# Kernel optimization log

Measured on AMD Instinct MI355X. Metric: run time of the kernel, lower is better.

## Reference

```python
import jax, jax.numpy as jnp
import numpy as np

B, S, E, DQ, DV = 8, 2048, 1024, 128, 128


def setup_inputs() -> dict:
    k0 = jax.random.key(0)
    ks = jax.random.split(k0, 10)
    scale_in = 1.0 / np.sqrt(E)
    return {
        "pad_mask": jax.random.uniform(ks[0], (B, S)) < 0.1,  # True = padded key position
        "query": jax.random.normal(ks[1], (B, S, E), jnp.float32),
        "key": jax.random.normal(ks[2], (B, S, E), jnp.float32),
        "value": jax.random.normal(ks[3], (B, S, E), jnp.float32),
        "Wq": jax.random.uniform(ks[4], (E, DQ), jnp.float32, -scale_in, scale_in),
        "bq": jnp.zeros((DQ,), jnp.float32),
        "Wk": jax.random.uniform(ks[5], (E, DQ), jnp.float32, -scale_in, scale_in),
        "bk": jnp.zeros((DQ,), jnp.float32),
        "Wv": jax.random.uniform(ks[6], (E, DV), jnp.float32, -scale_in, scale_in),
        "bv": jnp.zeros((DV,), jnp.float32),
    }


def reference(pad_mask, query, key, value, Wq, bq, Wk, bk, Wv, bv):
    # Linear projections (torch Linear: x @ W^T + b; weights stored pre-transposed here)
    q = query @ Wq + bq  # [B,S,DQ]
    k = key @ Wk + bk    # [B,S,DQ]
    v = value @ Wv + bv  # [B,S,DV]

    scores = jnp.einsum("bqd,bkd->bqk", q, k)  # [B,S,S]
    # Causal mask applied BEFORE scaling (as in source); -inf/scale is still -inf
    seq = scores.shape[1]
    causal = jnp.triu(jnp.ones((seq, seq), bool), k=1)
    scores = jnp.where(causal[None], -jnp.inf, scores)
    scores = scores / jnp.asarray(q.shape[-1] ** 0.5, scores.dtype)
    # Padding mask: mask key positions with -1e9 (broadcast over query dim)
    scores = jnp.where(pad_mask[:, None, :], jnp.asarray(-1e9, scores.dtype), scores)

    attn = jax.nn.softmax(scores, axis=-1)
    return jnp.einsum("bqk,bkd->bqd", attn, v)  # [B,S,DV]
```

## Files before the change

### kernel.cpp

```cpp
#include <hip/hip_runtime.h>
#include <hip/hip_bf16.h>

#define SEQ 2048
#define EMB 1024
#define DH  128
#define QSCALE 0.08838834764831845f

typedef __attribute__((ext_vector_type(4))) float f32x4;
typedef __attribute__((ext_vector_type(8))) short bf16x8;
typedef __attribute__((ext_vector_type(4))) short bf16x4;

__device__ __forceinline__ short f2bf(float f) {
  unsigned u = __builtin_bit_cast(unsigned, f);
  u += 0x7fffu + ((u >> 16) & 1u);
  return (short)(u >> 16);
}

__device__ __forceinline__ float bf2f(short s) {
  unsigned u = ((unsigned)(unsigned short)s) << 16;
  return __builtin_bit_cast(float, u);
}

__device__ __forceinline__ f32x4 mfma16(bf16x8 a, bf16x8 b, f32x4 c) {
  return __builtin_amdgcn_mfma_f32_16x16x32_bf16(a, b, c, 0, 0, 0);
}

__device__ __forceinline__ void gl_lds16(void* lds_base, const void* gsrc) {
  __builtin_amdgcn_global_load_lds(
      (const __attribute__((address_space(1))) void*)gsrc,
      (__attribute__((address_space(3))) void*)lds_base, 16, 0, 0);
}

__global__ void prep_weights(const float* __restrict__ Wq, const float* __restrict__ Wk,
                             const float* __restrict__ Wv, short* __restrict__ wt) {
  int gid = blockIdx.x * 256 + threadIdx.x;
  int lane = gid & 63, c = lane & 15, g = (lane >> 4) & 3;
  int nb = (gid >> 6) & 7;
  int kk = (gid >> 9) & 31;
  int p = gid >> 14;
  const float* W = (p == 0) ? Wq : ((p == 1) ? Wk : Wv);
  bf16x8 v;
#pragma unroll
  for (int j = 0; j < 8; ++j)
    v[j] = f2bf(W[(kk * 32 + g * 8 + j) * DH + nb * 16 + c]);
  *(bf16x8*)(&wt[(size_t)gid * 8]) = v;
}

__global__ __launch_bounds__(256, 2) void proj_gemm(
    const float* __restrict__ Xq, const float* __restrict__ Xk, const float* __restrict__ Xv,
    const short* __restrict__ wt,
    const float* __restrict__ bq, const float* __restrict__ bk, const float* __restrict__ bv,
    short* __restrict__ qp, short* __restrict__ kp, short* __restrict__ vt) {
  __shared__ char a_lds[4][2][8192];

  const int tid = threadIdx.x;
  const int w = tid >> 6, lane = tid & 63;
  const int g = lane >> 4, c = lane & 15;
  const int bid = blockIdx.x;
  const int p = bid >> 8, mb = bid & 255;
  const int row0 = (mb << 6) + (w << 4);
  const float* X    = (p == 0) ? Xq : ((p == 1) ? Xk : Xv);
  const float* bias = (p == 0) ? bq : ((p == 1) ? bk : bv);
  const char* Xs  = (const char*)X + (size_t)row0 * 4096;
  const char* WT  = (const char*)wt + (size_t)p * 262144;

  f32x4 acc[8];
#pragma unroll
  for (int nb = 0; nb < 8; ++nb) acc[nb] = (f32x4){0.f, 0.f, 0.f, 0.f};

  bf16x8 wr[2][8];

  auto stage_A = [&](int b, int kc) {
#pragma unroll
    for (int j = 0; j < 8; ++j) {
      int r = (j << 1) + (lane >> 5);
      int off = ((lane & 31) << 4) ^ ((r & 7) << 5);
      gl_lds16(&a_lds[w][b][j * 1024],
               Xs + (size_t)r * 4096 + kc * 512 + off);
    }
  };

  auto loadW = [&](bf16x8* dst, int t) {
#pragma unroll
    for (int nb = 0; nb < 8; ++nb)
      dst[nb] = *(const bf16x8*)(WT + (size_t)t * 8192 + nb * 1024 + (lane << 4));
  };

  auto computeT = [&](const bf16x8* wf, int b, int s) {
    const char* ab = &a_lds[w][b][0];
    int ad = (c << 9) + (((s << 7) + (g << 5)) ^ ((c & 7) << 5));
    f32x4 lo = *(const f32x4*)(ab + ad);
    f32x4 hi = *(const f32x4*)(ab + ad + 16);
    bf16x8 a;
#pragma unroll
    for (int j = 0; j < 4; ++j) { a[j] = f2bf(lo[j]); a[4 + j] = f2bf(hi[j]); }
#pragma unroll
    for (int nb = 0; nb < 8; ++nb) acc[nb] = mfma16(a, wf[nb], acc[nb]);
  };

  stage_A(0, 0);
  loadW(wr[0], 0);
  __builtin_amdgcn_sched_barrier(0);

#pragma unroll
  for (int t = 0; t < 32; ++t) {
    const int s = t & 3, kc = t >> 2;
    if (s == 0 && kc < 7) stage_A((kc + 1) & 1, kc + 1);
    if (t + 1 < 32) loadW(wr[(t + 1) & 1], t + 1);
    __builtin_amdgcn_sched_barrier(0);
    if (t == 31)                       asm volatile("s_waitcnt vmcnt(0)" ::: "memory");
    else if (s == 0 && t <= 24)        asm volatile("s_waitcnt vmcnt(16)" ::: "memory");
    else                               asm volatile("s_waitcnt vmcnt(8)" ::: "memory");
    __builtin_amdgcn_sched_barrier(0);
    computeT(wr[t & 1], kc & 1, s);
    __builtin_amdgcn_sched_barrier(0);
  }

  float bvals[8];
#pragma unroll
  for (int nb = 0; nb < 8; ++nb) bvals[nb] = bias[nb * 16 + c];

  if (p < 2) {
    short* outp = (p == 0) ? qp : kp;
    float sc = (p == 0) ? QSCALE : 1.0f;
#pragma unroll
    for (int r = 0; r < 4; ++r) {
      int token = row0 + g * 4 + r;
#pragma unroll
      for (int nb = 0; nb < 8; ++nb)
        outp[token * 128 + nb * 16 + c] = f2bf((acc[nb][r] + bvals[nb]) * sc);
    }
  } else {
    int tok0 = row0 + g * 4;
    int b_ = tok0 >> 11, s_ = tok0 & 2047;
#pragma unroll
    for (int nb = 0; nb < 8; ++nb) {
      int col = nb * 16 + c;
      bf16x4 v4;
#pragma unroll
      for (int r = 0; r < 4; ++r) v4[r] = f2bf(acc[nb][r] + bvals[nb]);
      *(bf16x4*)(&vt[((size_t)(b_ * 128 + col)) * 2048 + s_]) = v4;
    }
  }
}

__global__ __launch_bounds__(256) void avgv2_kernel(
    const short* __restrict__ vt, const int* __restrict__ pad,
    const float* __restrict__ bvv, float* __restrict__ avgv) {
  int b = blockIdx.x >> 3, dg = blockIdx.x & 7;
  int t = threadIdx.x, doff = t >> 4, sl = t & 15;
  int d = dg * 16 + doff;
  const short* vrow = vt + ((size_t)(b * 128 + d)) * 2048 + sl * 128;
  const int* prow = pad + (b << 11) + sl * 128;
  float sum = 0.f;
  int cnt = 0;
  for (int i = 0; i < 16; ++i) {
    bf16x8 v8 = *(const bf16x8*)(vrow + i * 8);
#pragma unroll
    for (int j = 0; j < 8; ++j) {
      int pd = prow[i * 8 + j];
      cnt += (pd != 0);
      if (pd) sum += bf2f(v8[j]);
    }
  }
#pragma unroll
  for (int xm = 1; xm < 16; xm <<= 1) {
    sum += __shfl_xor(sum, xm, 64);
    cnt += __shfl_xor(cnt, xm, 64);
  }
  if (sl == 0) avgv[(b << 7) + d] = (cnt > 0) ? (sum / (float)cnt) : 0.f;
  (void)bvv;
}

__device__ __forceinline__ void stage_kv(short* kb, short* vb,
                                         const char* kb_base, const char* vb_base,
                                         int kt, int w, int lane) {
#pragma unroll
  for (int ch = w; ch < 16; ch += 4) {
    int phys = ch * 1024 + lane * 16;
    int lg = phys ^ (((phys >> 8) & 7) << 4);
    gl_lds16((char*)kb + ch * 1024,
             kb_base + (size_t)(kt * 64 + (lg >> 8)) * 256 + (lg & 255));
  }
#pragma unroll
  for (int ch = w; ch < 16; ch += 4) {
    int phys = ch * 1024 + lane * 16;
    int lg = phys ^ (((phys >> 7) & 7) << 4);
    gl_lds16((char*)vb + ch * 1024,
             vb_base + (size_t)(lg >> 7) * 4096 + kt * 128 + (lg & 127));
  }
}

template <bool CAUSAL>
__device__ __forceinline__ void attn_tile(
    const short* __restrict__ k_lds, const short* __restrict__ v_lds, short* __restrict__ p_w,
    const bf16x8 (&qf)[4], f32x4 (&acc_o)[8], float (&m_r)[4], float (&l_r)[4],
    const int* __restrict__ padp, int kt, int qrow_g, int g, int c) {
  f32x4 sc[4];
#pragma unroll
  for (int nb = 0; nb < 4; ++nb) sc[nb] = (f32x4){0.f, 0.f, 0.f, 0.f};
#pragma unroll
  for (int ks = 0; ks < 4; ++ks) {
    bf16x8 kf[4];
#pragma unroll
    for (int nb = 0; nb < 4; ++nb) {
      int n = (nb << 4) + c;
      int off = (n << 8) + (ks << 6) + (g << 4);
      kf[nb] = *(const bf16x8*)((const char*)k_lds + (off ^ ((n & 7) << 4)));
    }
#pragma unroll
    for (int nb = 0; nb < 4; ++nb) sc[nb] = mfma16(qf[ks], kf[nb], sc[nb]);
  }

  int padv[4];
#pragma unroll
  for (int nb = 0; nb < 4; ++nb) padv[nb] = padp[kt + (nb << 4) + c];
  float sv[4][4];
#pragma unroll
  for (int nb = 0; nb < 4; ++nb) {
    bool pd = padv[nb] != 0;
    int key = kt + (nb << 4) + c;
#pragma unroll
    for (int r = 0; r < 4; ++r) {
      float s = sc[nb][r];
      if (CAUSAL && key > qrow_g + r) s = -1e30f;
      if (pd) s = -1e30f;
      sv[nb][r] = s;
    }
  }
  float tmax[4];
#pragma unroll
  for (int r = 0; r < 4; ++r)
    tmax[r] = fmaxf(fmaxf(sv[0][r], sv[1][r]), fmaxf(sv[2][r], sv[3][r]));
#pragma unroll
  for (int xm = 1; xm < 16; xm <<= 1)
#pragma unroll
    for (int r = 0; r < 4; ++r) tmax[r] = fmaxf(tmax[r], __shfl_xor(tmax[r], xm, 64));
  float al[4];
#pragma unroll
  for (int r = 0; r < 4; ++r) {
    float mn = fmaxf(m_r[r], tmax[r]);
    al[r] = __expf(m_r[r] - mn);
    m_r[r] = mn;
  }
  float ls[4] = {0.f, 0.f, 0.f, 0.f};
#pragma unroll
  for (int nb = 0; nb < 4; ++nb)
#pragma unroll
    for (int r = 0; r < 4; ++r) {
      float pp = __expf(sv[nb][r] - m_r[r]);
      sv[nb][r] = pp;
      ls[r] += pp;
    }
#pragma unroll
  for (int xm = 1; xm < 16; xm <<= 1)
#pragma unroll
    for (int r = 0; r < 4; ++r) ls[r] += __shfl_xor(ls[r], xm, 64);
#pragma unroll
  for (int r = 0; r < 4; ++r) l_r[r] = l_r[r] * al[r] + ls[r];
#pragma unroll
  for (int nb = 0; nb < 8; ++nb)
#pragma unroll
    for (int r = 0; r < 4; ++r) acc_o[nb][r] *= al[r];

#pragma unroll
  for (int nb = 0; nb < 4; ++nb)
#pragma unroll
    for (int r = 0; r < 4; ++r)
      p_w[(g * 4 + r) * 72 + (nb << 4) + c] = f2bf(sv[nb][r]);

#pragma unroll
  for (int ks = 0; ks < 2; ++ks) {
    bf16x8 pa = *(const bf16x8*)((const char*)p_w + c * 144 + ks * 64 + g * 16);
#pragma unroll
    for (int nb = 0; nb < 8; ++nb) {
      int n = (nb << 4) + c;
      int off = (n << 7) + (ks << 6) + (g << 4);
      bf16x8 vf = *(const bf16x8*)((const char*)v_lds + (off ^ ((n & 7) << 4)));
      acc_o[nb] = mfma16(pa, vf, acc_o[nb]);
    }
  }
}

__global__ __launch_bounds__(256) void flash_attn(
    const short* __restrict__ qp, const short* __restrict__ kp, const short* __restrict__ vt,
    const int* __restrict__ pad, float* __restrict__ partO, float* __restrict__ partML) {
  __shared__ short k_lds[2][64 * 128];
  __shared__ short v_lds[2][128 * 64];
  __shared__ short p_lds[4][16 * 72];
  const int tid = threadIdx.x, w = tid >> 6, lane = tid & 63;
  const int g = lane >> 4, c = lane & 15;
  const int j = blockIdx.x;
  int b, qi, half;
  if (j < 256) { b = j >> 5; qi = j & 31; half = 0; }
  else { int u = j - 256; b = u >> 5; qi = 31 - (u & 31); half = 1; }
  const int T = qi + 1;
  const int t0 = half ? (T >> 1) : 0;
  const int t1 = half ? T : (T >> 1);
  const int q0 = qi << 6;

  bf16x8 qf[4];
  {
    int token = (b << 11) + q0 + (w << 4) + c;
    const char* qrow = (const char*)qp + (size_t)token * 256;
#pragma unroll
    for (int s = 0; s < 4; ++s) qf[s] = *(const bf16x8*)(qrow + s * 64 + g * 16);
  }
  f32x4 acc_o[8];
#pragma unroll
  for (int i = 0; i < 8; ++i) acc_o[i] = (f32x4){0.f, 0.f, 0.f, 0.f};
  float m_r[4] = {-1e30f, -1e30f, -1e30f, -1e30f};
  float l_r[4] = {0.f, 0.f, 0.f, 0.f};

  const char* kb_base = (const char*)kp + (size_t)(b << 11) * 256;
  const char* vb_base = (const char*)vt + (size_t)b * 524288;
  const int* padp = pad + (b << 11);
  const int qrow_g = q0 + (w << 4) + (g << 2);

  if (t1 > t0) {
    stage_kv(k_lds[0], v_lds[0], kb_base, vb_base, t0, w, lane);
    __syncthreads();
    int cur = 0;
    for (int t = t0; t < t1; ++t) {
      if (t + 1 < t1)
        stage_kv(k_lds[cur ^ 1], v_lds[cur ^ 1], kb_base, vb_base, t + 1, w, lane);
      if (half && t == T - 1)
        attn_tile<true>(k_lds[cur], v_lds[cur], p_lds[w], qf, acc_o, m_r, l_r,
                        padp, t << 6, qrow_g, g, c);
      else
        attn_tile<false>(k_lds[cur], v_lds[cur], p_lds[w], qf, acc_o, m_r, l_r,
                         padp, t << 6, qrow_g, g, c);
      __syncthreads();
      cur ^= 1;
    }
  }

  float* pO = partO + (size_t)j * (64 * 128);
  float* pML = partML + (size_t)j * 128;
#pragma unroll
  for (int nb = 0; nb < 8; ++nb)
#pragma unroll
    for (int r = 0; r < 4; ++r)
      pO[(w * 16 + g * 4 + r) * 128 + (nb << 4) + c] = acc_o[nb][r];
  if (c == 0)
#pragma unroll
    for (int r = 0; r < 4; ++r) {
      pML[(w * 16 + g * 4 + r) * 2] = m_r[r];
      pML[(w * 16 + g * 4 + r) * 2 + 1] = l_r[r];
    }
}

__global__ __launch_bounds__(256) void combine_kernel(
    const float* __restrict__ partO, const float* __restrict__ partML,
    const float* __restrict__ avgv, float* __restrict__ out) {
  int gid = blockIdx.x * 256 + threadIdx.x;
  int row = gid >> 5;
  int d4 = gid & 31;
  int b = row >> 11, s = row & 2047;
  int qt = s >> 6, lr = s & 63;
  int wid1 = (b << 5) + qt;
  int wid2 = 256 + (b << 5) + (31 - qt);
  float m1 = partML[wid1 * 128 + lr * 2], l1 = partML[wid1 * 128 + lr * 2 + 1];
  float m2 = partML[wid2 * 128 + lr * 2], l2 = partML[wid2 * 128 + lr * 2 + 1];
  float m = fmaxf(m1, m2);
  f32x4 o;
  if (m < -1e8f) {
    o = *(const f32x4*)(avgv + (b << 7) + (d4 << 2));
  } else {
    float f1 = __expf(m1 - m), f2 = __expf(m2 - m);
    float inv = 1.0f / (l1 * f1 + l2 * f2);
    f32x4 o1 = *(const f32x4*)(partO + ((size_t)wid1 * 64 + lr) * 128 + (d4 << 2));
    f32x4 o2 = *(const f32x4*)(partO + ((size_t)wid2 * 64 + lr) * 128 + (d4 << 2));
#pragma unroll
    for (int k = 0; k < 4; ++k) o[k] = (o1[k] * f1 + o2[k] * f2) * inv;
  }
  *(f32x4*)(out + (size_t)row * 128 + (d4 << 2)) = o;
}

extern "C" void kernel_launch(void* const* d_in, const int* in_sizes, int n_in,
                              void* d_out, int out_size, void* d_ws, size_t ws_size,
                              hipStream_t stream) {
  const int*   pad   = (const int*)d_in[0];
  const float* query = (const float*)d_in[1];
  const float* key   = (const float*)d_in[2];
  const float* value = (const float*)d_in[3];
  const float* Wq    = (const float*)d_in[4];
  const float* bq    = (const float*)d_in[5];
  const float* Wk    = (const float*)d_in[6];
  const float* bk    = (const float*)d_in[7];
  const float* Wv    = (const float*)d_in[8];
  const float* bv    = (const float*)d_in[9];
  char* ws = (char*)d_ws;
  short* wt    = (short*)ws;
  short* qp    = (short*)(ws + 786432);
  short* kp    = (short*)(ws + 4980736);
  short* vt    = (short*)(ws + 9175040);
  float* partO = (float*)(ws + 13369344);
  float* partML= (float*)(ws + 30146560);
  float* avgv  = (float*)(ws + 30408704);
  float* out   = (float*)d_out;

  prep_weights<<<dim3(192), dim3(256), 0, stream>>>(Wq, Wk, Wv, wt);
  proj_gemm<<<dim3(768), dim3(256), 0, stream>>>(query, key, value, wt, bq, bk, bv, qp, kp, vt);
  avgv2_kernel<<<dim3(64), dim3(256), 0, stream>>>(vt, pad, bv, avgv);
  flash_attn<<<dim3(512), dim3(256), 0, stream>>>(qp, kp, vt, pad, partO, partML);
  combine_kernel<<<dim3(2048), dim3(256), 0, stream>>>(partO, partML, avgv, out);
}
```

Measured before the change: 105.6 us.

## Restructure projection GEMM into persistent blocks keeping weight slice in registers

The projection kernel becomes a persistent-style launch of 256 blocks of 8 waves. Each block walks 12 consecutive 16-row tiles, and each wave keeps its full 16-column weight slice (32 bf16x8 fragments) in registers, reloading only when the tile crosses into a different projection. The A tile is double-buffered in a 128KB LDS region shared across waves. This removes the repeated streaming of weights from global memory per K step. In exchange it adds block-wide barriers, much higher register and LDS pressure with only one block per CU, and a serial dependency chain of 32 MFMAs per tile.

```diff
diff --git a/kernel.cpp b/kernel.cpp
--- a/kernel.cpp
+++ b/kernel.cpp
@@ -46,99 +46,91 @@
   *(bf16x8*)(&wt[(size_t)gid * 8]) = v;
 }
 
-__global__ __launch_bounds__(256, 2) void proj_gemm(
+__global__ __launch_bounds__(512, 1) void proj_gemm(
     const float* __restrict__ Xq, const float* __restrict__ Xk, const float* __restrict__ Xv,
     const short* __restrict__ wt,
     const float* __restrict__ bq, const float* __restrict__ bk, const float* __restrict__ bv,
     short* __restrict__ qp, short* __restrict__ kp, short* __restrict__ vt) {
-  __shared__ char a_lds[4][2][8192];
+  __shared__ char a_lds[2][65536];
 
   const int tid = threadIdx.x;
   const int w = tid >> 6, lane = tid & 63;
   const int g = lane >> 4, c = lane & 15;
-  const int bid = blockIdx.x;
-  const int p = bid >> 8, mb = bid & 255;
-  const int row0 = (mb << 6) + (w << 4);
-  const float* X    = (p == 0) ? Xq : ((p == 1) ? Xk : Xv);
-  const float* bias = (p == 0) ? bq : ((p == 1) ? bk : bv);
-  const char* Xs  = (const char*)X + (size_t)row0 * 4096;
-  const char* WT  = (const char*)wt + (size_t)p * 262144;
-
-  f32x4 acc[8];
-#pragma unroll
-  for (int nb = 0; nb < 8; ++nb) acc[nb] = (f32x4){0.f, 0.f, 0.f, 0.f};
-
-  bf16x8 wr[2][8];
-
-  auto stage_A = [&](int b, int kc) {
-#pragma unroll
-    for (int j = 0; j < 8; ++j) {
-      int r = (j << 1) + (lane >> 5);
-      int off = ((lane & 31) << 4) ^ ((r & 7) << 5);
-      gl_lds16(&a_lds[w][b][j * 1024],
-               Xs + (size_t)r * 4096 + kc * 512 + off);
+  const int t0 = blockIdx.x * 12;
+
+  bf16x8 wr[32];
+  float bval = 0.f;
+
+  auto stageA = [&](int buf, int t) {
+    int pt = t >> 10, lt = t & 1023;
+    const float* X = (pt == 0) ? Xq : ((pt == 1) ? Xk : Xv);
+    const char* Xt = (const char*)X + (size_t)lt * 65536;
+#pragma unroll
+    for (int i = 0; i < 8; ++i) {
+      int id = (w << 3) | i;
+      int row = id >> 2, q = id & 3;
+      gl_lds16(a_lds[buf] + (row << 12) + (q << 10),
+               Xt + (row << 12) + (q << 10) + ((lane << 4) ^ ((row & 15) << 4)));
     }
   };
 
-  auto loadW = [&](bf16x8* dst, int t) {
-#pragma unroll
-    for (int nb = 0; nb < 8; ++nb)
-      dst[nb] = *(const bf16x8*)(WT + (size_t)t * 8192 + nb * 1024 + (lane << 4));
+  auto loadW = [&](int pt) {
+    const char* Wp = (const char*)wt + (size_t)pt * 262144 + (size_t)w * 1024 + (lane << 4);
+#pragma unroll
+    for (int kk = 0; kk < 32; ++kk)
+      wr[kk] = *(const bf16x8*)(Wp + (size_t)kk * 8192);
+    const float* bias = (pt == 0) ? bq : ((pt == 1) ? bk : bv);
+    bval = bias[(w << 4) + c];
   };
 
-  auto computeT = [&](const bf16x8* wf, int b, int s) {
-    const char* ab = &a_lds[w][b][0];
-    int ad = (c << 9) + (((s << 7) + (g << 5)) ^ ((c & 7) << 5));
-    f32x4 lo = *(const f32x4*)(ab + ad);
-    f32x4 hi = *(const f32x4*)(ab + ad + 16);
-    bf16x8 a;
-#pragma unroll
-    for (int j = 0; j < 4; ++j) { a[j] = f2bf(lo[j]); a[4 + j] = f2bf(hi[j]); }
-#pragma unroll
-    for (int nb = 0; nb < 8; ++nb) acc[nb] = mfma16(a, wf[nb], acc[nb]);
-  };
-
-  stage_A(0, 0);
-  loadW(wr[0], 0);
-  __builtin_amdgcn_sched_barrier(0);
-
-#pragma unroll
-  for (int t = 0; t < 32; ++t) {
-    const int s = t & 3, kc = t >> 2;
-    if (s == 0 && kc < 7) stage_A((kc + 1) & 1, kc + 1);
-    if (t + 1 < 32) loadW(wr[(t + 1) & 1], t + 1);
+  stageA(0, t0);
+  int cur_p = -1;
+
+#pragma unroll 1
+  for (int i = 0; i < 12; ++i) {
+    const int t = t0 + i;
+    const int pt = t >> 10;
+    __builtin_amdgcn_s_barrier();
+    if (i + 1 < 12) stageA((i + 1) & 1, t + 1);
+    const bool reload = (pt != cur_p);
+    if (reload) { loadW(pt); cur_p = pt; }
     __builtin_amdgcn_sched_barrier(0);
-    if (t == 31)                       asm volatile("s_waitcnt vmcnt(0)" ::: "memory");
-    else if (s == 0 && t <= 24)        asm volatile("s_waitcnt vmcnt(16)" ::: "memory");
-    else                               asm volatile("s_waitcnt vmcnt(8)" ::: "memory");
+    if (reload || i + 1 >= 12) asm volatile("s_waitcnt vmcnt(0)" ::: "memory");
+    else                       asm volatile("s_waitcnt vmcnt(8)" ::: "memory");
     __builtin_amdgcn_sched_barrier(0);
-    computeT(wr[t & 1], kc & 1, s);
+    __builtin_amdgcn_s_barrier();
+
+    f32x4 acc = (f32x4){0.f, 0.f, 0.f, 0.f};
+    const char* ab = a_lds[i & 1] + ((size_t)c << 12);
+#pragma unroll
+    for (int kk = 0; kk < 32; ++kk) {
+      int ad = ((kk << 7) + (g << 5)) ^ ((c & 15) << 4);
+      f32x4 lo = *(const f32x4*)(ab + ad);
+      f32x4 hi = *(const f32x4*)(ab + (ad ^ 16));
+      bf16x8 a;
+#pragma unroll
+      for (int j = 0; j < 4; ++j) { a[j] = f2bf(lo[j]); a[4 + j] = f2bf(hi[j]); }
+      acc = mfma16(a, wr[kk], acc);
+    }
     __builtin_amdgcn_sched_barrier(0);
-  }
-
-  float bvals[8];
-#pragma unroll
-  for (int nb = 0; nb < 8; ++nb) bvals[nb] = bias[nb * 16 + c];
-
-  if (p < 2) {
-    short* outp = (p == 0) ? qp : kp;
-    float sc = (p == 0) ? QSCALE : 1.0f;
-#pragma unroll
-    for (int r = 0; r < 4; ++r) {
-      int token = row0 + g * 4 + r;
-#pragma unroll
-      for (int nb = 0; nb < 8; ++nb)
-        outp[token * 128 + nb * 16 + c] = f2bf((acc[nb][r] + bvals[nb]) * sc);
-    }
-  } else {
-    int tok0 = row0 + g * 4;
-    int b_ = tok0 >> 11, s_ = tok0 & 2047;
-#pragma unroll
-    for (int nb = 0; nb < 8; ++nb) {
-      int col = nb * 16 + c;
+
+    const int lt = t & 1023;
+    const int row0 = lt << 4;
+    if (pt < 2) {
+      short* outp = (pt == 0) ? qp : kp;
+      float sc = (pt == 0) ? QSCALE : 1.0f;
+#pragma unroll
+      for (int r = 0; r < 4; ++r) {
+        int token = row0 + g * 4 + r;
+        outp[token * 128 + (w << 4) + c] = f2bf((acc[r] + bval) * sc);
+      }
+    } else {
+      int tok0 = row0 + g * 4;
+      int b_ = tok0 >> 11, s_ = tok0 & 2047;
+      int col = (w << 4) + c;
       bf16x4 v4;
 #pragma unroll
-      for (int r = 0; r < 4; ++r) v4[r] = f2bf(acc[nb][r] + bvals[nb]);
+      for (int r = 0; r < 4; ++r) v4[r] = f2bf(acc[r] + bval);
       *(bf16x4*)(&vt[((size_t)(b_ * 128 + col)) * 2048 + s_]) = v4;
     }
   }
@@ -401,7 +393,7 @@
   float* out   = (float*)d_out;
 
   prep_weights<<<dim3(192), dim3(256), 0, stream>>>(Wq, Wk, Wv, wt);
-  proj_gemm<<<dim3(768), dim3(256), 0, stream>>>(query, key, value, wt, bq, bk, bv, qp, kp, vt);
+  proj_gemm<<<dim3(256), dim3(512), 0, stream>>>(query, key, value, wt, bq, bk, bv, qp, kp, vt);
   avgv2_kernel<<<dim3(64), dim3(256), 0, stream>>>(vt, pad, bv, avgv);
   flash_attn<<<dim3(512), dim3(256), 0, stream>>>(qp, kp, vt, pad, partO, partML);
   combine_kernel<<<dim3(2048), dim3(256), 0, stream>>>(partO, partML, avgv, out);
```

Measured after the change: 233.2 us. 2.21x slower.
